# Optimization experiments

Hardware: AMD Instinct MI355X
Metric: run time of the kernel (lower is better)

## Reference

```python
import jax, jax.numpy as jnp
import numpy as np

EPS = 1e-5

def conv2d(x, w, b=None, pad=1):
    y = jax.lax.conv_general_dilated(x, w, (1, 1), [(pad, pad), (pad, pad)],
                                     dimension_numbers=('NCHW', 'OIHW', 'NCHW'))
    if b is not None:
        y = y + b[None, :, None, None]
    return y

def batchnorm(x, g, b):
    m = x.mean((0, 2, 3), keepdims=True)
    v = x.var((0, 2, 3), keepdims=True)
    return g[None, :, None, None] * (x - m) * jax.lax.rsqrt(v + EPS) + b[None, :, None, None]

def local_conv(x, w12):
    # x: [B,Ci,H,W]; w12: [B,Ci*9,H,W] -> per-pixel depthwise 3x3 conv
    B, Ci, H, W = x.shape
    xp = jnp.pad(x, ((0, 0), (0, 0), (1, 1), (1, 1)))
    patches = jnp.stack([xp[:, :, dh:dh + H, dw:dw + W]
                         for dh in range(3) for dw in range(3)], axis=2)  # [B,Ci,9,H,W]
    return (patches * w12.reshape(B, Ci, 9, H, W)).sum(axis=2)

def setup_inputs() -> dict:
    key = jax.random.key(0)
    ks = jax.random.split(key, 20)
    B, Ci, Cw, H, W = 4, 64, 64, 128, 128
    s = 0.05
    return {
        'input': jax.random.normal(ks[0], (B, Ci, H, W), jnp.float32),
        'weight': jax.random.normal(ks[1], (B, Cw, H, W), jnp.float32),
        'w_conv11': jax.random.normal(ks[2], (Ci, Ci + Cw, 3, 3), jnp.float32) * s,
        'b_conv11': jnp.zeros((Ci,), jnp.float32),
        'w_conv12': jax.random.normal(ks[3], (Ci * 9, Ci, 3, 3), jnp.float32) * s,
        'b_conv12': jnp.zeros((Ci * 9,), jnp.float32),
        'w_conv21': jax.random.normal(ks[4], (Ci, Ci + Cw, 3, 3), jnp.float32) * s,
        'b_conv21': jnp.zeros((Ci,), jnp.float32),
        'w_conv22': jax.random.normal(ks[5], (Ci * Ci, Ci, 1, 1), jnp.float32) * s,
        'b_conv22': jnp.zeros((Ci * Ci,), jnp.float32),
        'local_bn_g': jnp.ones((Ci,), jnp.float32),
        'local_bn_b': jnp.zeros((Ci,), jnp.float32),
        'br_g': jnp.ones((Ci,), jnp.float32),
        'br_b': jnp.zeros((Ci,), jnp.float32),
        'w_conv3': jax.random.normal(ks[6], (Ci, Ci, 3, 3), jnp.float32) * s,
        'conv3_bn_g': jnp.ones((Ci,), jnp.float32),
        'conv3_bn_b': jnp.zeros((Ci,), jnp.float32),
    }

def reference(input, weight, w_conv11, b_conv11, w_conv12, b_conv12,
              w_conv21, b_conv21, w_conv22, b_conv22,
              local_bn_g, local_bn_b, br_g, br_b,
              w_conv3, conv3_bn_g, conv3_bn_b):
    B, Ci, H, W = input.shape
    cat = jnp.concatenate([input, weight], axis=1)
    w11 = jax.nn.relu(conv2d(cat, w_conv11, b_conv11))
    w12 = conv2d(w11, w_conv12, b_conv12)                      # [B,Ci*9,H,W]
    w21 = jax.nn.relu(conv2d(cat, w_conv21, b_conv21))
    pooled = w21.mean((2, 3), keepdims=True)                   # [B,Ci,1,1]
    w22 = conv2d(pooled, w_conv22, b_conv22, pad=0).reshape(B, Ci, Ci)
    out1 = jax.nn.relu(batchnorm(local_conv(input, w12), local_bn_g, local_bn_b))
    out2 = jnp.einsum('bij,bjn->bin', w22, out1.reshape(B, Ci, H * W)).reshape(B, Ci, H, W)
    out3 = jax.nn.relu(batchnorm(out2, br_g, br_b))
    out4 = jax.nn.relu(batchnorm(conv2d(out3, w_conv3, None), conv3_bn_g, conv3_bn_b))
    return out4
```

## Files before the change

kernel.cpp:

```cpp
#include <hip/hip_runtime.h>

#define EPSV 1e-5f
#define HP 130
#define HW 16384

typedef unsigned int u32;
typedef unsigned short bfu;
typedef __bf16 bf16x8 __attribute__((ext_vector_type(8)));
typedef float  f32x4  __attribute__((ext_vector_type(4)));

__device__ __forceinline__ bfu f2bf(float f){
  u32 u = __builtin_bit_cast(u32, f);
  return (bfu)((u + 0x7FFFu + ((u >> 16) & 1u)) >> 16);
}
__device__ __forceinline__ float bf2f(bfu h){
  return __builtin_bit_cast(float, ((u32)h) << 16);
}
__device__ __forceinline__ f32x4 mfma16(bf16x8 a, bf16x8 b, f32x4 c){
  return __builtin_amdgcn_mfma_f32_16x16x32_bf16(a, b, c, 0, 0, 0);
}
__device__ __forceinline__ bf16x8 ldsfrag(const bfu* p){
  return __builtin_bit_cast(bf16x8, *(const uint4*)p);
}
__device__ __forceinline__ void gload_lds16(const uint4* g, uint4* l){
  __builtin_amdgcn_global_load_lds(
      (const __attribute__((address_space(1))) unsigned int*)g,
      (__attribute__((address_space(3))) unsigned int*)l, 16, 0, 0);
}


__global__ void k_zero_border(bfu* catT, bfu* w11T, bfu* out3T){
  int i = blockIdx.x*256 + threadIdx.x;
  if (i >= 4*516) return;
  int b = i/516, r = i - b*516;
  int hp, wpp;
  if (r < 130){ hp = 0; wpp = r; }
  else if (r < 260){ hp = 129; wpp = r - 130; }
  else { int r2 = r - 260; hp = 1 + (r2 >> 1); wpp = (r2 & 1)*129; }
  int pix = (b*HP + hp)*HP + wpp;
  uint4 z = {0,0,0,0};
  uint4* c4 = (uint4*)catT  + (size_t)pix*16;
  uint4* w4 = (uint4*)w11T  + (size_t)pix*8;
  uint4* o4 = (uint4*)out3T + (size_t)pix*8;
  #pragma unroll
  for (int k = 0; k < 16; ++k) c4[k] = z;
  #pragma unroll
  for (int k = 0; k < 8; ++k){ w4[k] = z; o4[k] = z; }
}

__global__ void k_prep_w(const float* __restrict__ w11w, const float* __restrict__ w21w,
                         const float* __restrict__ w12w, const float* __restrict__ w3w,
                         bfu* A11, bfu* A12, bfu* A3){
  const int total = 147456 + 331776 + 36864;
  for (int i = blockIdx.x*256 + threadIdx.x; i < total; i += gridDim.x*256){
    float v; bfu* dst;
    if (i < 147456){
      int tap = i >> 14, och = (i >> 7) & 127, cin = i & 127;
      v = (och < 64) ? w11w[(och*128 + cin)*9 + tap] : w21w[((och-64)*128 + cin)*9 + tap];
      dst = A11 + i;
    } else if (i < 147456 + 331776){
      int i2 = i - 147456;
      int g = i2 >> 12, t = g/9, tap2 = g%9;
      int c = (i2 >> 6) & 63, j = i2 & 63;
      v = w12w[((c*9 + t)*64 + j)*9 + tap2];
      dst = A12 + i2;
    } else {
      int i3 = i - (147456 + 331776);
      int tap2 = i3 >> 12, oc = (i3 >> 6) & 63, j = i3 & 63;
      v = w3w[(oc*64 + j)*9 + tap2];
      dst = A3 + i3;
    }
    *dst = f2bf(v);
  }
}

__global__ void k_prep_cat(const float* __restrict__ inp, const float* __restrict__ wgt, bfu* catT){
  __shared__ bfu lds[128*136];
  int b = blockIdx.y, h = blockIdx.x;
  int t = threadIdx.x;
  int w = t & 127, c0 = t >> 7;
  #pragma unroll 1
  for (int c = c0; c < 128; c += 2){
    const float* src = (c < 64) ? inp + ((b*64 + c)*128 + h)*128
                                : wgt + ((b*64 + (c-64))*128 + h)*128;
    lds[w*136 + c] = f2bf(src[w]);
  }
  __syncthreads();
  uint4* dst = (uint4*)catT;
  #pragma unroll
  for (int k = 0; k < 8; ++k){
    int idx = k*256 + t;
    int pix = idx >> 4, sub = idx & 15;
    uint4 v = *(const uint4*)&lds[pix*136 + sub*8];
    dst[(((b*HP + h+1)*HP) + (pix+1))*16 + sub] = v;
  }
}

__global__ __launch_bounds__(256) void k1_conv(
    const bfu* __restrict__ catT, const bfu* __restrict__ A11,
    const float* __restrict__ b11, const float* __restrict__ b21,
    bfu* __restrict__ w11T, float* __restrict__ poolP){
  __shared__ bfu lds[24480];
  int tid = threadIdx.x;
  int b = blockIdx.y, tile = blockIdx.x;
  int h0 = (tile >> 3)*8, w0 = (tile & 7)*16;

  const uint4* catT4 = (const uint4*)catT;
  for (int s = tid; s < 180*17; s += 256){
    int cell = s/17, sub = s%17;
    if (sub < 16){
      int th = cell/18, tw = cell%18;
      uint4 v = catT4[(((b*HP + h0+th)*HP) + (w0+tw))*16 + sub];
      *(uint4*)&lds[cell*136 + sub*8] = v;
    }
  }
  __syncthreads();

  int wid = tid >> 6, l = tid & 63, lg = l >> 4, pc = l & 15;
  int wm = wid >> 1, wn = wid & 1;
  f32x4 acc[4][4];
  #pragma unroll
  for (int i = 0; i < 4; ++i)
    #pragma unroll
    for (int j = 0; j < 4; ++j) acc[i][j] = f32x4{0.f,0.f,0.f,0.f};

  const uint4* A4 = (const uint4*)A11;
  #pragma unroll 3
  for (int tap = 0; tap < 9; ++tap){
    int kh = tap/3, kw = tap%3;
    #pragma unroll
    for (int jc = 0; jc < 4; ++jc){
      bf16x8 a[4], bb[4];
      #pragma unroll
      for (int fm = 0; fm < 4; ++fm){
        int row = wm*64 + fm*16 + pc;
        a[fm] = __builtin_bit_cast(bf16x8, A4[(tap*128 + row)*16 + jc*4 + lg]);
      }
      #pragma unroll
      for (int fn = 0; fn < 4; ++fn){
        int cell = (wn*4 + fn + kh)*18 + (pc + kw);
        bb[fn] = ldsfrag(&lds[cell*136 + jc*32 + lg*8]);
      }
      #pragma unroll
      for (int fm = 0; fm < 4; ++fm)
        #pragma unroll
        for (int fn = 0; fn < 4; ++fn)
          acc[fm][fn] = mfma16(a[fm], bb[fn], acc[fm][fn]);
    }
  }
  __syncthreads();

  if (wm == 0){
    #pragma unroll
    for (int fm = 0; fm < 4; ++fm)
      #pragma unroll
      for (int r = 0; r < 4; ++r){
        int och = fm*16 + lg*4 + r;
        float bias = b11[och];
        #pragma unroll
        for (int fn = 0; fn < 4; ++fn){
          float v = acc[fm][fn][r] + bias;
          v = v > 0.f ? v : 0.f;
          int px = wn*64 + fn*16 + pc;
          lds[px*72 + och] = f2bf(v);
        }
      }
  } else {
    float* statsF = (float*)&lds[20000];
    #pragma unroll
    for (int fm = 0; fm < 4; ++fm)
      #pragma unroll
      for (int r = 0; r < 4; ++r){
        int cw = fm*16 + lg*4 + r;
        float bias = b21[cw];
        float s = 0.f;
        #pragma unroll
        for (int fn = 0; fn < 4; ++fn){
          float v = acc[fm][fn][r] + bias;
          s += (v > 0.f ? v : 0.f);
        }
        s += __shfl_xor(s,1); s += __shfl_xor(s,2); s += __shfl_xor(s,4); s += __shfl_xor(s,8);
        if (pc == 0) statsF[wn*64 + cw] = s;
      }
  }
  __syncthreads();

  if (wid < 2){
    int px = tid;
    int h = h0 + (px >> 4), w = w0 + (px & 15);
    uint4* dst = (uint4*)w11T + (((b*HP + h+1)*HP) + (w+1))*8;
    const uint4* srcT = (const uint4*)&lds[px*72];
    #pragma unroll
    for (int k = 0; k < 8; ++k) dst[k] = srcT[k];
  }
  if (tid < 64){
    float* statsF = (float*)&lds[20000];
    poolP[(b*128 + tile)*64 + tid] = statsF[tid] + statsF[64 + tid];
  }
}

__global__ void k2a_pool(const float* __restrict__ poolP, float* pooled){
  int t = threadIdx.x;
  int b = t >> 6, c = t & 63;
  float s = 0.f;
  for (int tile = 0; tile < 128; ++tile) s += poolP[(b*128 + tile)*64 + c];
  pooled[t] = s * (1.f/16384.f);
}

__global__ void k2b_w22(const float* __restrict__ pooled, const float* __restrict__ W22,
                        const float* __restrict__ b22, bfu* __restrict__ w22bf){
  __shared__ float pl[64];
  int b = blockIdx.x >> 4, og = blockIdx.x & 15;
  if (threadIdx.x < 64) pl[threadIdx.x] = pooled[b*64 + threadIdx.x];
  __syncthreads();
  int o = og*256 + threadIdx.x;
  float acc = b22[o];
  #pragma unroll 4
  for (int c = 0; c < 64; ++c) acc += pl[c]*W22[o*64 + c];
  w22bf[b*4096 + o] = f2bf(acc);
}

__global__ __launch_bounds__(256) void k3_fused(
    const bfu* __restrict__ w11T, const bfu* __restrict__ catT,
    const bfu* __restrict__ A12, const float* __restrict__ b12,
    float* __restrict__ out1, float* __restrict__ outP){
  __shared__ bfu ldsW[324*64];
  __shared__ bfu ldsA[2*4096];
  __shared__ float b12f[576];
  int tid = threadIdx.x;
  int b = blockIdx.y, tile = blockIdx.x, g = blockIdx.z;
  int h0 = (tile >> 3)*16, w0 = (tile & 7)*16;
  int base = g ? 5 : 0;
  int ns   = g ? 4 : 5;
  float* outp = g ? outP : out1;

  int wid = tid >> 6, l = tid & 63, lg = l >> 4, pc = l & 15;
  int w4 = wid*4;

  const uint4* A4 = (const uint4*)A12;
  uint4* ldsA4 = (uint4*)ldsA;
  int srcA = ((tid >> 7)*16 + (tid & 15))*8 + ((tid >> 6) & 1)*4 + ((tid >> 4) & 3);
  uint4* dstBase = ldsA4 + wid*64;

  {
    const uint4* sb = A4 + (size_t)base*512 + srcA;
    gload_lds16(sb,       dstBase);
    gload_lds16(sb + 256, dstBase + 256);
  }

  const uint4* w11T4 = (const uint4*)w11T;
  for (int s = tid; s < 324*8; s += 256){
    int cell = s >> 3, sub = s & 7;
    int th = cell/18, tw = cell - th*18;
    uint4 v = w11T4[(((b*HP + h0+th)*HP) + (w0+tw))*8 + sub];
    *(uint4*)&ldsW[cell*64 + ((sub*8) ^ ((cell&7)<<3))] = v;
  }
  for (int i = tid; i < 576; i += 256) b12f[i] = b12[i];
  __syncthreads();

  f32x4 oacc[4][4];
  #pragma unroll
  for (int i = 0; i < 4; ++i)
    #pragma unroll
    for (int j = 0; j < 4; ++j) oacc[i][j] = f32x4{0.f,0.f,0.f,0.f};
  f32x4 y[4][4];
  int cur = 0, tt = 0, s = 0;
  const int NQ = ns*9;

  #pragma unroll 1
  for (int q = 0; q < NQ; ++q){
    if (q + 1 < NQ){
      int s1 = s + 1, tt1 = tt;
      if (s1 == ns){ s1 = 0; ++tt1; }
      const uint4* sb = A4 + (size_t)(tt1*9 + base + s1)*512 + srcA;
      uint4* db = ldsA4 + (cur^1)*512 + wid*64;
      gload_lds16(sb,       db);
      gload_lds16(sb + 256, db + 256);
    }
    if (s == 0){
      #pragma unroll
      for (int i = 0; i < 4; ++i)
        #pragma unroll
        for (int j = 0; j < 4; ++j) y[i][j] = f32x4{0.f,0.f,0.f,0.f};
    }
    int tap2 = base + s;
    int kh = (tap2 >= 6) ? 2 : ((tap2 >= 3) ? 1 : 0);
    int kw = tap2 - kh*3;
    #pragma unroll
    for (int jc = 0; jc < 2; ++jc){
      bf16x8 a[4], bbf[4];
      #pragma unroll
      for (int fm = 0; fm < 4; ++fm)
        a[fm] = __builtin_bit_cast(bf16x8, ldsA4[cur*512 + (fm*2 + jc)*64 + l]);
      #pragma unroll
      for (int fn = 0; fn < 4; ++fn){
        int cell = (w4 + fn + kh)*18 + (pc + kw);
        bbf[fn] = ldsfrag(&ldsW[cell*64 + ((jc*32 + lg*8) ^ ((cell&7)<<3))]);
      }
      #pragma unroll
      for (int fm = 0; fm < 4; ++fm)
        #pragma unroll
        for (int fn = 0; fn < 4; ++fn)
          y[fm][fn] = mfma16(a[fm], bbf[fn], y[fm][fn]);
    }
    __syncthreads();

    if (s == ns - 1){
      int dh = (tt >= 6) ? 2 : ((tt >= 3) ? 1 : 0);
      int dw = tt - dh*3;
      #pragma unroll
      for (int fn = 0; fn < 4; ++fn){
        const bfu* bp = catT + ((size_t)((b*HP + h0 + w4 + fn + dh)*HP) + (w0 + pc + dw))*128 + lg*4;
        #pragma unroll
        for (int fm = 0; fm < 4; ++fm){
          ushort4 iv = *(const ushort4*)(bp + fm*16);
          float i0 = bf2f(iv.x), i1 = bf2f(iv.y), i2 = bf2f(iv.z), i3 = bf2f(iv.w);
          int c = fm*16 + lg*4;
          float bz0 = g ? 0.f : b12f[(c+0)*9 + tt];
          float bz1 = g ? 0.f : b12f[(c+1)*9 + tt];
          float bz2 = g ? 0.f : b12f[(c+2)*9 + tt];
          float bz3 = g ? 0.f : b12f[(c+3)*9 + tt];
          oacc[fm][fn][0] += i0 * (y[fm][fn][0] + bz0);
          oacc[fm][fn][1] += i1 * (y[fm][fn][1] + bz1);
          oacc[fm][fn][2] += i2 * (y[fm][fn][2] + bz2);
          oacc[fm][fn][3] += i3 * (y[fm][fn][3] + bz3);
        }
      }
    }
    ++s; if (s == ns){ s = 0; ++tt; }
    cur ^= 1;
  }

  #pragma unroll
  for (int fm = 0; fm < 4; ++fm)
    #pragma unroll
    for (int r = 0; r < 4; ++r){
      int c = fm*16 + lg*4 + r;
      #pragma unroll
      for (int fn = 0; fn < 4; ++fn)
        outp[((b*64 + c)*128 + h0 + w4 + fn)*128 + (w0 + pc)] = oacc[fm][fn][r];
    }
}

__global__ __launch_bounds__(256) void k3b_stat(
    const float* __restrict__ out1, const float* __restrict__ outP, float* __restrict__ st){
  __shared__ float red[8];
  int bc = blockIdx.x, t = threadIdx.x;
  const float4* p1 = (const float4*)(out1 + (size_t)bc*HW);
  const float4* p2 = (const float4*)(outP + (size_t)bc*HW);
  float s = 0.f, ss = 0.f;
  #pragma unroll 4
  for (int i = t; i < 4096; i += 256){
    float4 a = p1[i], q = p2[i];
    float v0 = a.x+q.x, v1 = a.y+q.y, v2 = a.z+q.z, v3 = a.w+q.w;
    s  += v0+v1+v2+v3;
    ss += v0*v0+v1*v1+v2*v2+v3*v3;
  }
  #pragma unroll
  for (int m = 1; m < 64; m <<= 1){ s += __shfl_xor(s, m); ss += __shfl_xor(ss, m); }
  if ((t & 63) == 0){ red[(t >> 6)*2] = s; red[(t >> 6)*2 + 1] = ss; }
  __syncthreads();
  if (t == 0){
    s  = red[0] + red[2] + red[4] + red[6];
    ss = red[1] + red[3] + red[5] + red[7];
    st[bc*2] = s; st[bc*2 + 1] = ss;
  }
}

__global__ void k_bnstat(const float* __restrict__ st, int nblk, float n,
                         const float* __restrict__ g, const float* __restrict__ bb, float* bn){
  __shared__ float red[512];
  int tid = threadIdx.x;
  int c = tid & 63, kk = tid >> 6;
  float s = 0.f, ss = 0.f;
  for (int k = kk; k < nblk; k += 4){
    float2 v = *(const float2*)&st[(k*64 + c)*2];
    s += v.x; ss += v.y;
  }
  red[tid*2] = s; red[tid*2 + 1] = ss;
  __syncthreads();
  if (tid < 64){
    #pragma unroll
    for (int q = 1; q < 4; ++q){ s += red[(q*64 + tid)*2]; ss += red[(q*64 + tid)*2 + 1]; }
    float mean = s/n, var = ss/n - mean*mean;
    float a = g[tid]*rsqrtf(var + EPSV);
    bn[tid*2] = a; bn[tid*2 + 1] = bb[tid] - mean*a;
  }
}

__global__ __launch_bounds__(256) void k4_einsum(
    const float* __restrict__ out1, const float* __restrict__ outP,
    const bfu* __restrict__ w22bf, const float* __restrict__ bn1,
    float* __restrict__ out2, float* __restrict__ st2){
  __shared__ bfu ldsX[256*72];
  __shared__ float a1[64], be1[64];
  __shared__ float wp[512];
  int tid = threadIdx.x;
  int b = blockIdx.y, chunk = blockIdx.x;
  if (tid < 64){ a1[tid] = bn1[tid*2]; be1[tid] = bn1[tid*2 + 1]; }
  __syncthreads();
  int p0 = chunk*256;

  {
    int px = tid;
    const float* src1 = out1 + (size_t)(b*64)*HW + p0 + px;
    const float* src2 = outP + (size_t)(b*64)*HW + p0 + px;
    #pragma unroll 1
    for (int j0 = 0; j0 < 64; j0 += 4){
      float x0 = src1[(j0+0)*HW] + src2[(j0+0)*HW]; x0 = a1[j0+0]*x0 + be1[j0+0]; x0 = x0 > 0.f ? x0 : 0.f;
      float x1 = src1[(j0+1)*HW] + src2[(j0+1)*HW]; x1 = a1[j0+1]*x1 + be1[j0+1]; x1 = x1 > 0.f ? x1 : 0.f;
      float x2 = src1[(j0+2)*HW] + src2[(j0+2)*HW]; x2 = a1[j0+2]*x2 + be1[j0+2]; x2 = x2 > 0.f ? x2 : 0.f;
      float x3 = src1[(j0+3)*HW] + src2[(j0+3)*HW]; x3 = a1[j0+3]*x3 + be1[j0+3]; x3 = x3 > 0.f ? x3 : 0.f;
      ushort4 pk; pk.x = f2bf(x0); pk.y = f2bf(x1); pk.z = f2bf(x2); pk.w = f2bf(x3);
      *(ushort4*)&ldsX[px*72 + j0] = pk;
    }
  }
  __syncthreads();

  int wid = tid >> 6, l = tid & 63, lg = l >> 4, pc = l & 15;
  const uint4* W4 = (const uint4*)w22bf;
  f32x4 acc[4][4];
  #pragma unroll
  for (int i = 0; i < 4; ++i)
    #pragma unroll
    for (int j = 0; j < 4; ++j) acc[i][j] = f32x4{0.f,0.f,0.f,0.f};

  #pragma unroll
  for (int jc = 0; jc < 2; ++jc){
    bf16x8 a[4], bb[4];
    #pragma unroll
    for (int fm = 0; fm < 4; ++fm)
      a[fm] = __builtin_bit_cast(bf16x8, W4[b*512 + (fm*16 + pc)*8 + jc*4 + lg]);
    #pragma unroll
    for (int fn = 0; fn < 4; ++fn)
      bb[fn] = ldsfrag(&ldsX[(wid*64 + fn*16 + pc)*72 + jc*32 + lg*8]);
    #pragma unroll
    for (int fm = 0; fm < 4; ++fm)
      #pragma unroll
      for (int fn = 0; fn < 4; ++fn)
        acc[fm][fn] = mfma16(a[fm], bb[fn], acc[fm][fn]);
  }

  #pragma unroll
  for (int fm = 0; fm < 4; ++fm)
    #pragma unroll
    for (int r = 0; r < 4; ++r){
      int i = fm*16 + lg*4 + r;
      float s = 0.f, ss = 0.f;
      #pragma unroll
      for (int fn = 0; fn < 4; ++fn){
        int px = wid*64 + fn*16 + pc;
        float v = acc[fm][fn][r];
        out2[(b*64 + i)*HW + p0 + px] = v;
        s += v; ss += v*v;
      }
      s += __shfl_xor(s,1); s += __shfl_xor(s,2); s += __shfl_xor(s,4); s += __shfl_xor(s,8);
      ss += __shfl_xor(ss,1); ss += __shfl_xor(ss,2); ss += __shfl_xor(ss,4); ss += __shfl_xor(ss,8);
      if (pc == 0){ wp[(wid*64 + i)*2] = s; wp[(wid*64 + i)*2 + 1] = ss; }
    }
  __syncthreads();
  if (tid < 64){
    float s = 0.f, ss = 0.f;
    #pragma unroll
    for (int w = 0; w < 4; ++w){ s += wp[(w*64 + tid)*2]; ss += wp[(w*64 + tid)*2 + 1]; }
    int blin = b*64 + chunk;
    st2[(blin*64 + tid)*2] = s; st2[(blin*64 + tid)*2 + 1] = ss;
  }
}

__global__ void k4c_out3(const float* __restrict__ out2, const float* __restrict__ bn2, bfu* out3T){
  __shared__ bfu lds[128*72];
  int b = blockIdx.y, h = blockIdx.x;
  int t = threadIdx.x;
  int px = t & 127, ch = (t >> 7)*32;
  #pragma unroll 1
  for (int cc = 0; cc < 32; cc += 4){
    int c = ch + cc;
    float x0 = out2[((b*64 + c+0) << 14) + (h << 7) + px];
    float x1 = out2[((b*64 + c+1) << 14) + (h << 7) + px];
    float x2 = out2[((b*64 + c+2) << 14) + (h << 7) + px];
    float x3 = out2[((b*64 + c+3) << 14) + (h << 7) + px];
    x0 = bn2[(c+0)*2]*x0 + bn2[(c+0)*2+1]; x0 = x0 > 0.f ? x0 : 0.f;
    x1 = bn2[(c+1)*2]*x1 + bn2[(c+1)*2+1]; x1 = x1 > 0.f ? x1 : 0.f;
    x2 = bn2[(c+2)*2]*x2 + bn2[(c+2)*2+1]; x2 = x2 > 0.f ? x2 : 0.f;
    x3 = bn2[(c+3)*2]*x3 + bn2[(c+3)*2+1]; x3 = x3 > 0.f ? x3 : 0.f;
    ushort4 pk; pk.x = f2bf(x0); pk.y = f2bf(x1); pk.z = f2bf(x2); pk.w = f2bf(x3);
    *(ushort4*)&lds[px*72 + c] = pk;
  }
  __syncthreads();
  uint4* dst = (uint4*)out3T;
  #pragma unroll
  for (int k = 0; k < 4; ++k){
    int idx = k*256 + t;
    int pix = idx >> 3, sub = idx & 7;
    uint4 v = *(const uint4*)&lds[pix*72 + sub*8];
    dst[((size_t)(b*HP + h+1)*HP + (pix+1))*8 + sub] = v;
  }
}

__global__ __launch_bounds__(256) void k5_conv3(
    const bfu* __restrict__ out3T, const bfu* __restrict__ A3,
    float* __restrict__ outc, float* __restrict__ st3){
  __shared__ bfu lds[180*72];
  __shared__ float wp[512];
  int tid = threadIdx.x;
  int b = blockIdx.y, tile = blockIdx.x;
  int h0 = (tile >> 3)*8, w0 = (tile & 7)*16;
  const uint4* src4 = (const uint4*)out3T;
  for (int s = tid; s < 180*8; s += 256){
    int cell = s >> 3, sub = s & 7;
    int th = cell/18, tw = cell - th*18;
    *(uint4*)&lds[cell*72 + sub*8] = src4[(((b*HP + h0+th)*HP) + (w0+tw))*8 + sub];
  }
  __syncthreads();

  int wid = tid >> 6, l = tid & 63, lg = l >> 4, pc = l & 15;
  f32x4 acc[4][2];
  #pragma unroll
  for (int i = 0; i < 4; ++i){ acc[i][0] = f32x4{0.f,0.f,0.f,0.f}; acc[i][1] = f32x4{0.f,0.f,0.f,0.f}; }
  const uint4* A4 = (const uint4*)A3;
  #pragma unroll 3
  for (int tap2 = 0; tap2 < 9; ++tap2){
    int kh = tap2/3, kw = tap2 - kh*3;
    #pragma unroll
    for (int jc = 0; jc < 2; ++jc){
      bf16x8 a[4], bb[2];
      #pragma unroll
      for (int fm = 0; fm < 4; ++fm)
        a[fm] = __builtin_bit_cast(bf16x8, A4[tap2*512 + (fm*16 + pc)*8 + jc*4 + lg]);
      #pragma unroll
      for (int fn = 0; fn < 2; ++fn){
        int cell = (wid*2 + fn + kh)*18 + (pc + kw);
        bb[fn] = ldsfrag(&lds[cell*72 + jc*32 + lg*8]);
      }
      #pragma unroll
      for (int fm = 0; fm < 4; ++fm)
        #pragma unroll
        for (int fn = 0; fn < 2; ++fn)
          acc[fm][fn] = mfma16(a[fm], bb[fn], acc[fm][fn]);
    }
  }
  #pragma unroll
  for (int fm = 0; fm < 4; ++fm)
    #pragma unroll
    for (int r = 0; r < 4; ++r){
      int c = fm*16 + lg*4 + r;
      float s = 0.f, ss = 0.f;
      #pragma unroll
      for (int fn = 0; fn < 2; ++fn){
        int pr = wid*2 + fn;
        float v = acc[fm][fn][r];
        outc[((b*64 + c)*128 + h0 + pr)*128 + (w0 + pc)] = v;
        s += v; ss += v*v;
      }
      s += __shfl_xor(s,1); s += __shfl_xor(s,2); s += __shfl_xor(s,4); s += __shfl_xor(s,8);
      ss += __shfl_xor(ss,1); ss += __shfl_xor(ss,2); ss += __shfl_xor(ss,4); ss += __shfl_xor(ss,8);
      if (pc == 0){ wp[(wid*64 + c)*2] = s; wp[(wid*64 + c)*2 + 1] = ss; }
    }
  __syncthreads();
  if (tid < 64){
    float s = 0.f, ss = 0.f;
    #pragma unroll
    for (int w = 0; w < 4; ++w){ s += wp[(w*64 + tid)*2]; ss += wp[(w*64 + tid)*2 + 1]; }
    int blin = b*128 + tile;
    st3[(blin*64 + tid)*2] = s; st3[(blin*64 + tid)*2 + 1] = ss;
  }
}

__global__ void k6_final(float4* __restrict__ out, const float* __restrict__ bn3){
  const int total4 = 4*64*HW/4;
  for (int i = blockIdx.x*256 + threadIdx.x; i < total4; i += gridDim.x*256){
    int c = (i >> 12) & 63;
    float a = bn3[c*2], be = bn3[c*2 + 1];
    float4 x = out[i];
    x.x = a*x.x + be; x.x = x.x > 0.f ? x.x : 0.f;
    x.y = a*x.y + be; x.y = x.y > 0.f ? x.y : 0.f;
    x.z = a*x.z + be; x.z = x.z > 0.f ? x.z : 0.f;
    x.w = a*x.w + be; x.w = x.w > 0.f ? x.w : 0.f;
    out[i] = x;
  }
}

extern "C" void kernel_launch(void* const* d_in, const int* in_sizes, int n_in,
                              void* d_out, int out_size, void* d_ws, size_t ws_size,
                              hipStream_t stream){
  const float* inp  = (const float*)d_in[0];
  const float* wgt  = (const float*)d_in[1];
  const float* w11w = (const float*)d_in[2];
  const float* b11  = (const float*)d_in[3];
  const float* w12w = (const float*)d_in[4];
  const float* b12  = (const float*)d_in[5];
  const float* w21w = (const float*)d_in[6];
  const float* b21  = (const float*)d_in[7];
  const float* W22  = (const float*)d_in[8];
  const float* b22  = (const float*)d_in[9];
  const float* lg   = (const float*)d_in[10];
  const float* lb   = (const float*)d_in[11];
  const float* brg  = (const float*)d_in[12];
  const float* brb  = (const float*)d_in[13];
  const float* w3w  = (const float*)d_in[14];
  const float* c3g  = (const float*)d_in[15];
  const float* c3b  = (const float*)d_in[16];

  if (ws_size < 53200000) return;

  char* ws = (char*)d_ws;
  bfu*   catT  = (bfu*)(ws);
  bfu*   w11T  = (bfu*)(ws + 17305600);
  bfu*   out3T = (bfu*)(ws + 25958400);
  bfu*   A11   = (bfu*)(ws + 34611200);
  bfu*   A12   = (bfu*)(ws + 34906112);
  bfu*   A3    = (bfu*)(ws + 35569664);
  float* out1  = (float*)(ws + 35643392);
  float* poolP = (float*)(ws + 52420608);
  float* pooled= (float*)(ws + 52551680);
  bfu*   w22bf = (bfu*)(ws + 52552704);
  float* st13  = (float*)(ws + 52585472);
  float* bn1   = (float*)(ws + 52847616);
  float* st2   = (float*)(ws + 52848128);
  float* bn2   = (float*)(ws + 52979200);
  float* bn3   = (float*)(ws + 52979712);
  float* outF  = (float*)d_out;

  k_zero_border<<<dim3(9),  dim3(256), 0, stream>>>(catT, w11T, out3T);
  k_prep_w  <<<dim3(512),  dim3(256), 0, stream>>>(w11w, w21w, w12w, w3w, A11, A12, A3);
  k_prep_cat<<<dim3(128,4),dim3(256), 0, stream>>>(inp, wgt, catT);
  k1_conv   <<<dim3(128,4),dim3(256), 0, stream>>>(catT, A11, b11, b21, w11T, poolP);
  k2a_pool  <<<dim3(1),    dim3(256), 0, stream>>>(poolP, pooled);
  k2b_w22   <<<dim3(64),   dim3(256), 0, stream>>>(pooled, W22, b22, w22bf);
  k3_fused  <<<dim3(64,4,2),dim3(256),0, stream>>>(w11T, catT, A12, b12, out1, outF);
  k3b_stat  <<<dim3(256),  dim3(256), 0, stream>>>(out1, outF, st13);
  k_bnstat  <<<dim3(1),    dim3(256), 0, stream>>>(st13, 4, 65536.f, lg, lb, bn1);
  k4_einsum <<<dim3(64,4), dim3(256), 0, stream>>>(out1, outF, w22bf, bn1, outF, st2);
  k_bnstat  <<<dim3(1),    dim3(256), 0, stream>>>(st2, 256, 65536.f, brg, brb, bn2);
  k4c_out3  <<<dim3(128,4),dim3(256), 0, stream>>>(outF, bn2, out3T);
  k5_conv3  <<<dim3(128,4),dim3(256), 0, stream>>>(out3T, A3, outF, st13);
  k_bnstat  <<<dim3(1),    dim3(256), 0, stream>>>(st13, 512, 65536.f, c3g, c3b, bn3);
  k6_final  <<<dim3(1024), dim3(256), 0, stream>>>((float4*)outF, bn3);
}
```

Baseline: 321.4 us.

## Stage conv11 weights in LDS with double buffering; split conv12 by channel half

In k1_conv, the A11 weight fragments were read directly from global memory inside the MFMA loop. They are now prefetched into double-buffered LDS with async global-to-LDS loads. The cat tile is stored with an XOR swizzle in place of the padded stride. In k3_fused, the two z-blocks no longer split the 9 taps 5/4; each now takes half of the 64 input channels over all taps, with three taps staged per iteration. This changes load balance, how much of w11T and the weights each block loads, and the number of barriers per block.

```diff
diff --git a/kernel.cpp b/kernel.cpp
--- a/kernel.cpp
+++ b/kernel.cpp
@@ -100,46 +100,69 @@
     const bfu* __restrict__ catT, const bfu* __restrict__ A11,
     const float* __restrict__ b11, const float* __restrict__ b21,
     bfu* __restrict__ w11T, float* __restrict__ poolP){
-  __shared__ bfu lds[24480];
+  __shared__ bfu ldsC[180*128];
+  __shared__ bfu ldsA[2*8192];
+  __shared__ float statsF[128];
   int tid = threadIdx.x;
   int b = blockIdx.y, tile = blockIdx.x;
   int h0 = (tile >> 3)*8, w0 = (tile & 7)*16;
 
-  const uint4* catT4 = (const uint4*)catT;
-  for (int s = tid; s < 180*17; s += 256){
-    int cell = s/17, sub = s%17;
-    if (sub < 16){
-      int th = cell/18, tw = cell%18;
-      uint4 v = catT4[(((b*HP + h0+th)*HP) + (w0+tw))*16 + sub];
-      *(uint4*)&lds[cell*136 + sub*8] = v;
-    }
-  }
-  __syncthreads();
-
   int wid = tid >> 6, l = tid & 63, lg = l >> 4, pc = l & 15;
   int wm = wid >> 1, wn = wid & 1;
+  int pcT = tid & 15, lgT = (tid >> 4) & 3;
+
+  const uint4* A4 = (const uint4*)A11;
+  uint4* ldsA4 = (uint4*)ldsA;
+
+  #pragma unroll
+  for (int k = 0; k < 4; ++k){
+    int q = k*4 + wid;
+    int row = (q >> 1)*16 + pcT;
+    gload_lds16(A4 + row*16 + (q&1)*4 + lgT, ldsA4 + k*256 + wid*64);
+  }
+
+  const uint4* catT4 = (const uint4*)catT;
+  for (int s = tid; s < 180*16; s += 256){
+    int cell = s >> 4, sub = s & 15;
+    int th = cell/18, tw = cell - th*18;
+    uint4 v = catT4[(((b*HP + h0+th)*HP) + (w0+tw))*16 + sub];
+    *(uint4*)&ldsC[cell*128 + ((sub*8) ^ ((cell&7)<<3))] = v;
+  }
+  __syncthreads();
+
   f32x4 acc[4][4];
   #pragma unroll
   for (int i = 0; i < 4; ++i)
     #pragma unroll
     for (int j = 0; j < 4; ++j) acc[i][j] = f32x4{0.f,0.f,0.f,0.f};
 
-  const uint4* A4 = (const uint4*)A11;
-  #pragma unroll 3
-  for (int tap = 0; tap < 9; ++tap){
-    int kh = tap/3, kw = tap%3;
-    #pragma unroll
-    for (int jc = 0; jc < 4; ++jc){
+  int cur = 0;
+  #pragma unroll 1
+  for (int cc = 0; cc < 18; ++cc){
+    int tap = cc >> 1, p = cc & 1;
+    if (cc < 17){
+      int cc1 = cc + 1, tap1 = cc1 >> 1, p1 = cc1 & 1;
+      #pragma unroll
+      for (int k = 0; k < 4; ++k){
+        int q = k*4 + wid;
+        int row = (q >> 1)*16 + pcT;
+        gload_lds16(A4 + tap1*2048 + row*16 + p1*8 + (q&1)*4 + lgT,
+                    ldsA4 + (cur^1)*1024 + k*256 + wid*64);
+      }
+    }
+    int kh = (tap >= 6) ? 2 : ((tap >= 3) ? 1 : 0);
+    int kw = tap - kh*3;
+    #pragma unroll
+    for (int jq = 0; jq < 2; ++jq){
+      int jc = p*2 + jq;
       bf16x8 a[4], bb[4];
       #pragma unroll
-      for (int fm = 0; fm < 4; ++fm){
-        int row = wm*64 + fm*16 + pc;
-        a[fm] = __builtin_bit_cast(bf16x8, A4[(tap*128 + row)*16 + jc*4 + lg]);
-      }
+      for (int fm = 0; fm < 4; ++fm)
+        a[fm] = __builtin_bit_cast(bf16x8, ldsA4[cur*1024 + ((wm*4 + fm)*2 + jq)*64 + l]);
       #pragma unroll
       for (int fn = 0; fn < 4; ++fn){
         int cell = (wn*4 + fn + kh)*18 + (pc + kw);
-        bb[fn] = ldsfrag(&lds[cell*136 + jc*32 + lg*8]);
+        bb[fn] = ldsfrag(&ldsC[cell*128 + ((jc*32 + lg*8) ^ ((cell&7)<<3))]);
       }
       #pragma unroll
       for (int fm = 0; fm < 4; ++fm)
@@ -147,8 +170,9 @@
         for (int fn = 0; fn < 4; ++fn)
           acc[fm][fn] = mfma16(a[fm], bb[fn], acc[fm][fn]);
     }
-  }
-  __syncthreads();
+    __syncthreads();
+    cur ^= 1;
+  }
 
   if (wm == 0){
     #pragma unroll
@@ -162,11 +186,10 @@
           float v = acc[fm][fn][r] + bias;
           v = v > 0.f ? v : 0.f;
           int px = wn*64 + fn*16 + pc;
-          lds[px*72 + och] = f2bf(v);
+          ldsC[px*72 + och] = f2bf(v);
         }
       }
   } else {
-    float* statsF = (float*)&lds[20000];
     #pragma unroll
     for (int fm = 0; fm < 4; ++fm)
       #pragma unroll
@@ -189,14 +212,12 @@
     int px = tid;
     int h = h0 + (px >> 4), w = w0 + (px & 15);
     uint4* dst = (uint4*)w11T + (((b*HP + h+1)*HP) + (w+1))*8;
-    const uint4* srcT = (const uint4*)&lds[px*72];
+    const uint4* srcT = (const uint4*)&ldsC[px*72];
     #pragma unroll
     for (int k = 0; k < 8; ++k) dst[k] = srcT[k];
   }
-  if (tid < 64){
-    float* statsF = (float*)&lds[20000];
+  if (tid < 64)
     poolP[(b*128 + tile)*64 + tid] = statsF[tid] + statsF[64 + tid];
-  }
 }
 
 __global__ void k2a_pool(const float* __restrict__ poolP, float* pooled){
@@ -225,34 +246,32 @@
     const bfu* __restrict__ A12, const float* __restrict__ b12,
     float* __restrict__ out1, float* __restrict__ outP){
   __shared__ bfu ldsW[324*64];
-  __shared__ bfu ldsA[2*4096];
+  __shared__ bfu ldsA[2*3*2048];
   __shared__ float b12f[576];
   int tid = threadIdx.x;
   int b = blockIdx.y, tile = blockIdx.x, g = blockIdx.z;
   int h0 = (tile >> 3)*16, w0 = (tile & 7)*16;
-  int base = g ? 5 : 0;
-  int ns   = g ? 4 : 5;
-  float* outp = g ? outP : out1;
 
   int wid = tid >> 6, l = tid & 63, lg = l >> 4, pc = l & 15;
   int w4 = wid*4;
+  int g4 = g*4;
+  float* outp = g ? outP : out1;
 
   const uint4* A4 = (const uint4*)A12;
   uint4* ldsA4 = (uint4*)ldsA;
-  int srcA = ((tid >> 7)*16 + (tid & 15))*8 + ((tid >> 6) & 1)*4 + ((tid >> 4) & 3);
+  int srcA = ((tid >> 6)*16 + (tid & 15))*8 + g4 + ((tid >> 4) & 3);
   uint4* dstBase = ldsA4 + wid*64;
 
-  {
-    const uint4* sb = A4 + (size_t)base*512 + srcA;
-    gload_lds16(sb,       dstBase);
-    gload_lds16(sb + 256, dstBase + 256);
-  }
+  #pragma unroll
+  for (int s = 0; s < 3; ++s)
+    gload_lds16(A4 + (size_t)s*512 + srcA, dstBase + s*256);
 
   const uint4* w11T4 = (const uint4*)w11T;
-  for (int s = tid; s < 324*8; s += 256){
-    int cell = s >> 3, sub = s & 7;
+  for (int s = tid; s < 324*4; s += 256){
+    int cell = s >> 2, q = s & 3;
     int th = cell/18, tw = cell - th*18;
-    uint4 v = w11T4[(((b*HP + h0+th)*HP) + (w0+tw))*8 + sub];
+    uint4 v = w11T4[(((b*HP + h0+th)*HP) + (w0+tw))*8 + g4 + q];
+    int sub = g4 + q;
     *(uint4*)&ldsW[cell*64 + ((sub*8) ^ ((cell&7)<<3))] = v;
   }
   for (int i = tid; i < 576; i += 256) b12f[i] = b12[i];
@@ -264,38 +283,35 @@
     #pragma unroll
     for (int j = 0; j < 4; ++j) oacc[i][j] = f32x4{0.f,0.f,0.f,0.f};
   f32x4 y[4][4];
-  int cur = 0, tt = 0, s = 0;
-  const int NQ = ns*9;
+  int cur = 0;
+  int boff = g*32 + lg*8;
 
   #pragma unroll 1
-  for (int q = 0; q < NQ; ++q){
-    if (q + 1 < NQ){
-      int s1 = s + 1, tt1 = tt;
-      if (s1 == ns){ s1 = 0; ++tt1; }
-      const uint4* sb = A4 + (size_t)(tt1*9 + base + s1)*512 + srcA;
-      uint4* db = ldsA4 + (cur^1)*512 + wid*64;
-      gload_lds16(sb,       db);
-      gload_lds16(sb + 256, db + 256);
-    }
-    if (s == 0){
+  for (int cc = 0; cc < 27; ++cc){
+    int tt = cc/3, m3 = cc - tt*3;
+    if (cc < 26){
+      const uint4* sb = A4 + (size_t)((cc+1)*3)*512 + srcA;
+      uint4* db = ldsA4 + (cur^1)*768 + wid*64;
+      #pragma unroll
+      for (int s = 0; s < 3; ++s)
+        gload_lds16(sb + s*512, db + s*256);
+    }
+    if (m3 == 0){
       #pragma unroll
       for (int i = 0; i < 4; ++i)
         #pragma unroll
         for (int j = 0; j < 4; ++j) y[i][j] = f32x4{0.f,0.f,0.f,0.f};
     }
-    int tap2 = base + s;
-    int kh = (tap2 >= 6) ? 2 : ((tap2 >= 3) ? 1 : 0);
-    int kw = tap2 - kh*3;
-    #pragma unroll
-    for (int jc = 0; jc < 2; ++jc){
+    #pragma unroll
+    for (int t3 = 0; t3 < 3; ++t3){
       bf16x8 a[4], bbf[4];
       #pragma unroll
       for (int fm = 0; fm < 4; ++fm)
-        a[fm] = __builtin_bit_cast(bf16x8, ldsA4[cur*512 + (fm*2 + jc)*64 + l]);
+        a[fm] = __builtin_bit_cast(bf16x8, ldsA4[cur*768 + t3*256 + fm*64 + l]);
       #pragma unroll
       for (int fn = 0; fn < 4; ++fn){
-        int cell = (w4 + fn + kh)*18 + (pc + kw);
-        bbf[fn] = ldsfrag(&ldsW[cell*64 + ((jc*32 + lg*8) ^ ((cell&7)<<3))]);
+        int cell = (w4 + fn + m3)*18 + (pc + t3);
+        bbf[fn] = ldsfrag(&ldsW[cell*64 + (boff ^ ((cell&7)<<3))]);
       }
       #pragma unroll
       for (int fm = 0; fm < 4; ++fm)
@@ -304,10 +320,8 @@
           y[fm][fn] = mfma16(a[fm], bbf[fn], y[fm][fn]);
     }
     __syncthreads();
-
-    if (s == ns - 1){
-      int dh = (tt >= 6) ? 2 : ((tt >= 3) ? 1 : 0);
-      int dw = tt - dh*3;
+    if (m3 == 2){
+      int dh = tt/3, dw = tt - dh*3;
       #pragma unroll
       for (int fn = 0; fn < 4; ++fn){
         const bfu* bp = catT + ((size_t)((b*HP + h0 + w4 + fn + dh)*HP) + (w0 + pc + dw))*128 + lg*4;
@@ -327,7 +341,6 @@
         }
       }
     }
-    ++s; if (s == ns){ s = 0; ++tt; }
     cur ^= 1;
   }
 
```

Measured after the change: 295.5 us (median of 2 runs). 1.09x faster.
